# Kernel tuning notes

Measured on AMD Instinct MI355X. Metric: run time of the kernel, lower is better.

The kernel has to match this reference:

```python
import jax, jax.numpy as jnp
import numpy as np

N_NODES = 100000
D_SRC = 128
D_DST = 128
D_OUT = 256
N_EDGES = 600000


def setup_inputs() -> dict:
    key = jax.random.key(0)
    k1, k2, k3, k4, k5 = jax.random.split(key, 5)
    x_src = jax.random.normal(k1, (N_NODES, D_SRC), dtype=jnp.float32)
    x_dst = jax.random.normal(k2, (N_NODES, D_DST), dtype=jnp.float32)
    edge_index = jax.random.randint(k3, (2, N_EDGES), 0, N_NODES, dtype=jnp.int64)
    # Linear(in_src + in_dst, out): torch stores W as [out, in]
    fan_in = D_SRC + D_DST
    bound = 1.0 / np.sqrt(fan_in)
    W = jax.random.uniform(k4, (D_OUT, fan_in), minval=-bound, maxval=bound, dtype=jnp.float32)
    b = jax.random.uniform(k5, (D_OUT,), minval=-bound, maxval=bound, dtype=jnp.float32)
    return {"x_src": x_src, "x_dst": x_dst, "edge_index": edge_index, "W": W, "b": b}


def reference(x_src, x_dst, edge_index, W, b):
    src_idx, dst_idx = edge_index[0], edge_index[1]
    n_dst = x_dst.shape[0]
    x_j = x_src[src_idx]                                  # [E, D_SRC] gather
    summed = jax.ops.segment_sum(x_j, dst_idx, num_segments=n_dst)   # [N, D_SRC]
    count = jax.ops.segment_sum(jnp.ones((src_idx.shape[0],), dtype=x_src.dtype),
                                dst_idx, num_segments=n_dst)          # [N]
    agg = summed / jnp.maximum(count, 1.0)[:, None]        # scatter-mean
    h = jnp.concatenate([x_dst, agg], axis=-1)             # [N, D_DST+D_SRC]
    return jax.nn.relu(h @ W.T + b)                        # [N, D_OUT]
```

## Files before the change

### kernel.cpp

```cpp
#include <hip/hip_runtime.h>

#define N_NODES 100000
#define D_SRC 128
#define D_OUT 256
#define K_DIM 256
#define CAP 32
#define OVF_CAP 2048

typedef __attribute__((ext_vector_type(8))) short short8;
typedef __attribute__((ext_vector_type(4))) float float4v;

__device__ inline unsigned short f2bf(float f) {
    unsigned int u = __float_as_uint(f);
    u += 0x7FFF + ((u >> 16) & 1);
    return (unsigned short)(u >> 16);
}
__device__ inline float bf_lo(unsigned int u) { return __uint_as_float(u << 16); }
__device__ inline float bf_hi(unsigned int u) { return __uint_as_float(u & 0xFFFF0000u); }

__global__ __launch_bounds__(256) void bucket_kernel(
    const int* __restrict__ ei,
    int* __restrict__ deg,
    int* __restrict__ ovf_cnt,
    int* __restrict__ ovf,
    int* __restrict__ bucket,
    int n_edges)
{
    int e = blockIdx.x * 256 + threadIdx.x;
    if (e >= n_edges) return;
    int s = ei[e];
    int d = ei[n_edges + e];
    int pos = atomicAdd(deg + d, 1);
    if (pos < CAP) {
        bucket[(size_t)d * CAP + pos] = s;
    } else {
        int o = atomicAdd(ovf_cnt, 1);
        if (o < OVF_CAP) { ovf[2 * o] = s; ovf[2 * o + 1] = d; }
    }
}

__global__ __launch_bounds__(256) void pack_src_kernel(
    const float* __restrict__ x, unsigned short* __restrict__ xb)
{
    int i = blockIdx.x * 256 + threadIdx.x;
    float4 v = ((const float4*)x)[i];
    ushort4 o;
    o.x = f2bf(v.x); o.y = f2bf(v.y); o.z = f2bf(v.z); o.w = f2bf(v.w);
    ((ushort4*)xb)[i] = o;
}

__global__ __launch_bounds__(256) void pack_dst_sw_kernel(
    const float* __restrict__ x, unsigned short* __restrict__ xdsw)
{
    int t = blockIdx.x * 256 + threadIdx.x;
    int r = t >> 4;
    int g = t & 15;
    const float4* p = (const float4*)(x + (size_t)r * 128 + g * 8);
    float4 v0 = p[0], v1 = p[1];
    union { unsigned short s[8]; short8 v; } pk;
    pk.s[0] = f2bf(v0.x); pk.s[1] = f2bf(v0.y);
    pk.s[2] = f2bf(v0.z); pk.s[3] = f2bf(v0.w);
    pk.s[4] = f2bf(v1.x); pk.s[5] = f2bf(v1.y);
    pk.s[6] = f2bf(v1.z); pk.s[7] = f2bf(v1.w);
    size_t gr = ((size_t)(r >> 4) * 4 + (g >> 2)) * 64 + (r & 15) + ((g & 3) << 4);
    ((short8*)xdsw)[gr] = pk.v;
}

__global__ __launch_bounds__(256) void convert_w_sw_kernel(
    const float* __restrict__ W, unsigned short* __restrict__ wsw)
{
    int t = blockIdx.x * 256 + threadIdx.x;
    int r = t >> 5;
    int g = t & 31;
    const float4* p = (const float4*)(W + (size_t)r * 256 + g * 8);
    float4 v0 = p[0], v1 = p[1];
    union { unsigned short s[8]; short8 v; } pk;
    pk.s[0] = f2bf(v0.x); pk.s[1] = f2bf(v0.y);
    pk.s[2] = f2bf(v0.z); pk.s[3] = f2bf(v0.w);
    pk.s[4] = f2bf(v1.x); pk.s[5] = f2bf(v1.y);
    pk.s[6] = f2bf(v1.z); pk.s[7] = f2bf(v1.w);
    size_t gr = ((size_t)(r >> 4) * 8 + (g >> 2)) * 64 + (r & 15) + ((g & 3) << 4);
    ((short8*)wsw)[gr] = pk.v;
}

__global__ __launch_bounds__(256) void gather_kernel(
    const unsigned short* __restrict__ xsb,
    const int*   __restrict__ deg,
    const int*   __restrict__ bucket,
    const int*   __restrict__ ovf_cnt,
    const int*   __restrict__ ovf,
    unsigned int* __restrict__ aggsw)
{
    int node = blockIdx.x * 4 + (threadIdx.x >> 6);
    if (node >= N_NODES) return;
    int lane = threadIdx.x & 63;

    int dtot = deg[node];
    int n = (dtot < CAP) ? dtot : CAP;

    int idx = bucket[(size_t)node * CAP + (lane & 31)];

    float ax = 0.f, ay = 0.f;
    int i = 0;
    for (; i + 4 <= n; i += 4) {
        int s0 = __shfl(idx, i);
        int s1 = __shfl(idx, i + 1);
        int s2 = __shfl(idx, i + 2);
        int s3 = __shfl(idx, i + 3);
        unsigned int u0 = ((const unsigned int*)(xsb + (size_t)s0 * D_SRC))[lane];
        unsigned int u1 = ((const unsigned int*)(xsb + (size_t)s1 * D_SRC))[lane];
        unsigned int u2 = ((const unsigned int*)(xsb + (size_t)s2 * D_SRC))[lane];
        unsigned int u3 = ((const unsigned int*)(xsb + (size_t)s3 * D_SRC))[lane];
        ax += bf_lo(u0) + bf_lo(u1) + bf_lo(u2) + bf_lo(u3);
        ay += bf_hi(u0) + bf_hi(u1) + bf_hi(u2) + bf_hi(u3);
    }
    for (; i < n; ++i) {
        int s0 = __shfl(idx, i);
        unsigned int u0 = ((const unsigned int*)(xsb + (size_t)s0 * D_SRC))[lane];
        ax += bf_lo(u0);
        ay += bf_hi(u0);
    }

    if (dtot > CAP) {
        int oc = *ovf_cnt;
        if (oc > OVF_CAP) oc = OVF_CAP;
        for (int o = 0; o < oc; ++o) {
            if (ovf[2 * o + 1] == node) {
                int s0 = ovf[2 * o];
                unsigned int u0 = ((const unsigned int*)(xsb + (size_t)s0 * D_SRC))[lane];
                ax += bf_lo(u0);
                ay += bf_hi(u0);
            }
        }
    }

    float inv = 1.0f / (float)((dtot > 1) ? dtot : 1);
    unsigned int packed = (unsigned int)f2bf(ax * inv)
                        | ((unsigned int)f2bf(ay * inv) << 16);
    size_t dw = ((size_t)(node >> 4) * 4 + (lane >> 4)) * 256
              + (size_t)((node & 15) + 16 * ((lane >> 2) & 3)) * 4 + (lane & 3);
    aggsw[dw] = packed;
}

__global__ __launch_bounds__(256) void mfma_gemm_kernel(
    const short8* __restrict__ xdsw,
    const short8* __restrict__ aggsw,
    const short8* __restrict__ wsw,
    const float* __restrict__ bias,
    float*       __restrict__ out)
{
    __shared__ float eps[4][16][68];

    int wave = threadIdx.x >> 6;
    int lane = threadIdx.x & 63;
    int lrow = lane & 15;
    int kq   = lane >> 4;
    int mb   = blockIdx.x;
    int m0   = mb * 64;
    int n0   = wave * 64;

    bool mok[4];
    #pragma unroll
    for (int mf = 0; mf < 4; ++mf) mok[mf] = (m0 + mf * 16) < N_NODES;

    const short8* Ax = xdsw  + (size_t)mb * 1024 + lane;
    const short8* Ag = aggsw + (size_t)mb * 1024 + lane;
    const short8* Bw = wsw   + (size_t)wave * 2048 + lane;

    float4v acc[4][4];
    #pragma unroll
    for (int i = 0; i < 4; ++i)
        #pragma unroll
        for (int j = 0; j < 4; ++j)
            acc[i][j] = (float4v){0.f, 0.f, 0.f, 0.f};

    const short8 zfrag = (short8){0,0,0,0,0,0,0,0};
    short8 a[2][4], b[2][4];

    #pragma unroll
    for (int mf = 0; mf < 4; ++mf)
        a[0][mf] = mok[mf] ? Ax[mf * 256] : zfrag;
    #pragma unroll
    for (int nf = 0; nf < 4; ++nf)
        b[0][nf] = Bw[nf * 512];

    #pragma unroll
    for (int kc = 0; kc < 8; ++kc) {
        const int cur = kc & 1, nxt = cur ^ 1;
        if (kc < 7) {
            const int k1 = kc + 1;
            const short8* A = (k1 < 4) ? Ax : Ag;
            const int kk = (k1 < 4) ? k1 : (k1 - 4);
            #pragma unroll
            for (int mf = 0; mf < 4; ++mf)
                a[nxt][mf] = mok[mf] ? A[mf * 256 + kk * 64] : zfrag;
            #pragma unroll
            for (int nf = 0; nf < 4; ++nf)
                b[nxt][nf] = Bw[nf * 512 + k1 * 64];
        }
        #pragma unroll
        for (int mf = 0; mf < 4; ++mf)
            #pragma unroll
            for (int nf = 0; nf < 4; ++nf)
                acc[mf][nf] = __builtin_amdgcn_mfma_f32_16x16x32_bf16(
                    a[cur][mf], b[cur][nf], acc[mf][nf], 0, 0, 0);
    }

    float bv[4];
    #pragma unroll
    for (int nf = 0; nf < 4; ++nf)
        bv[nf] = bias[n0 + nf * 16 + lrow];

    int srow   = lane >> 4;
    int schunk = lane & 15;

    #pragma unroll
    for (int mf = 0; mf < 4; ++mf) {
        if (!mok[mf]) continue;
        #pragma unroll
        for (int nf = 0; nf < 4; ++nf)
            #pragma unroll
            for (int r = 0; r < 4; ++r)
                eps[wave][kq * 4 + r][nf * 16 + lrow] =
                    fmaxf(acc[mf][nf][r] + bv[nf], 0.f);
        asm volatile("s_waitcnt lgkmcnt(0)" ::: "memory");
        #pragma unroll
        for (int c = 0; c < 4; ++c) {
            int row  = c * 4 + srow;
            float4 v = *(const float4*)&eps[wave][row][schunk * 4];
            int grow = m0 + mf * 16 + row;
            *(float4*)(out + (size_t)grow * D_OUT + n0 + schunk * 4) = v;
        }
        asm volatile("s_waitcnt lgkmcnt(0)" ::: "memory");
    }
}

extern "C" void kernel_launch(void* const* d_in, const int* in_sizes, int n_in,
                              void* d_out, int out_size, void* d_ws, size_t ws_size,
                              hipStream_t stream) {
    const float* x_src = (const float*)d_in[0];
    const float* x_dst = (const float*)d_in[1];
    const int*   ei    = (const int*)d_in[2];
    const float* W     = (const float*)d_in[3];
    const float* bias  = (const float*)d_in[4];
    float* out = (float*)d_out;

    int n_edges = in_sizes[2] / 2;

    int* deg     = (int*)d_ws;
    int* ovf_cnt = deg + N_NODES;
    int* ovf     = ovf_cnt + 4;
    unsigned short* wsw   = (unsigned short*)(ovf + OVF_CAP * 2);
    unsigned short* aggsw = wsw + (size_t)D_OUT * K_DIM;
    unsigned short* xdsw  = aggsw + (size_t)(N_NODES / 16) * 4 * 64 * 8;

    int* bucket = (int*)d_out;
    unsigned short* xsb = (unsigned short*)(bucket + (size_t)N_NODES * CAP);

    hipMemsetAsync(d_ws, 0, (N_NODES + 4) * sizeof(int), stream);

    bucket_kernel<<<(n_edges + 255) / 256, 256, 0, stream>>>(
        ei, deg, ovf_cnt, ovf, bucket, n_edges);

    pack_src_kernel<<<(N_NODES * D_SRC / 4) / 256, 256, 0, stream>>>(x_src, xsb);

    pack_dst_sw_kernel<<<(N_NODES * 16) / 256, 256, 0, stream>>>(x_dst, xdsw);

    convert_w_sw_kernel<<<(D_OUT * K_DIM / 8) / 256, 256, 0, stream>>>(W, wsw);

    gather_kernel<<<(N_NODES + 3) / 4, 256, 0, stream>>>(
        xsb, deg, bucket, ovf_cnt, ovf, (unsigned int*)aggsw);

    mfma_gemm_kernel<<<(N_NODES + 63) / 64, 256, 0, stream>>>(
        (const short8*)xdsw, (const short8*)aggsw, (const short8*)wsw, bias, out);
}
```

Baseline: 314.4 us.

## Merge prep kernels and memset, batch gather loads, use nontemporal output stores

The x_src pack, x_dst swizzled pack, W conversion and degree-counter zeroing now run as one block-partitioned prep kernel, replacing three launches plus a memset. The gather loop issues up to eight predicated row loads before accumulating, to keep more memory requests in flight per wave. The GEMM epilogue writes output with nontemporal stores so the large output stream does not pollute cache. The trade-offs are extra predicated work when degrees are low and possible cache-behaviour shifts, since the output buffer is also reused as scratch earlier in the pipeline.

```diff
diff --git a/kernel.cpp b/kernel.cpp
--- a/kernel.cpp
+++ b/kernel.cpp
@@ -17,6 +17,61 @@
 }
 __device__ inline float bf_lo(unsigned int u) { return __uint_as_float(u << 16); }
 __device__ inline float bf_hi(unsigned int u) { return __uint_as_float(u & 0xFFFF0000u); }
+
+#define PREP_SRC_BLOCKS 12500
+#define PREP_DST_BLOCKS 6250
+#define PREP_W_BLOCKS   32
+#define PREP_Z_BLOCKS   98
+#define PREP_BLOCKS (PREP_SRC_BLOCKS + PREP_DST_BLOCKS + PREP_W_BLOCKS + PREP_Z_BLOCKS)
+
+__global__ __launch_bounds__(256) void prep_kernel(
+    const float* __restrict__ x_src,
+    const float* __restrict__ x_dst,
+    const float* __restrict__ W,
+    unsigned short* __restrict__ xsb,
+    unsigned short* __restrict__ xdsw,
+    unsigned short* __restrict__ wsw,
+    int* __restrict__ deg)
+{
+    int b = blockIdx.x;
+    if (b < PREP_SRC_BLOCKS) {
+        int i = b * 256 + threadIdx.x;
+        float4 v = ((const float4*)x_src)[i];
+        ushort4 o;
+        o.x = f2bf(v.x); o.y = f2bf(v.y); o.z = f2bf(v.z); o.w = f2bf(v.w);
+        ((ushort4*)xsb)[i] = o;
+    } else if (b < PREP_SRC_BLOCKS + PREP_DST_BLOCKS) {
+        int t = (b - PREP_SRC_BLOCKS) * 256 + threadIdx.x;
+        int r = t >> 4;
+        int g = t & 15;
+        const float4* p = (const float4*)(x_dst + (size_t)r * 128 + g * 8);
+        float4 v0 = p[0], v1 = p[1];
+        union { unsigned short s[8]; short8 v; } pk;
+        pk.s[0] = f2bf(v0.x); pk.s[1] = f2bf(v0.y);
+        pk.s[2] = f2bf(v0.z); pk.s[3] = f2bf(v0.w);
+        pk.s[4] = f2bf(v1.x); pk.s[5] = f2bf(v1.y);
+        pk.s[6] = f2bf(v1.z); pk.s[7] = f2bf(v1.w);
+        size_t gr = ((size_t)(r >> 4) * 4 + (g >> 2)) * 64 + (r & 15) + ((g & 3) << 4);
+        ((short8*)xdsw)[gr] = pk.v;
+    } else if (b < PREP_SRC_BLOCKS + PREP_DST_BLOCKS + PREP_W_BLOCKS) {
+        int t = (b - PREP_SRC_BLOCKS - PREP_DST_BLOCKS) * 256 + threadIdx.x;
+        int r = t >> 5;
+        int g = t & 31;
+        const float4* p = (const float4*)(W + (size_t)r * 256 + g * 8);
+        float4 v0 = p[0], v1 = p[1];
+        union { unsigned short s[8]; short8 v; } pk;
+        pk.s[0] = f2bf(v0.x); pk.s[1] = f2bf(v0.y);
+        pk.s[2] = f2bf(v0.z); pk.s[3] = f2bf(v0.w);
+        pk.s[4] = f2bf(v1.x); pk.s[5] = f2bf(v1.y);
+        pk.s[6] = f2bf(v1.z); pk.s[7] = f2bf(v1.w);
+        size_t gr = ((size_t)(r >> 4) * 8 + (g >> 2)) * 64 + (r & 15) + ((g & 3) << 4);
+        ((short8*)wsw)[gr] = pk.v;
+    } else {
+        int i = (b - PREP_SRC_BLOCKS - PREP_DST_BLOCKS - PREP_W_BLOCKS) * 256 + threadIdx.x;
+        if (i < (N_NODES + 4) / 4)
+            ((int4*)deg)[i] = make_int4(0, 0, 0, 0);
+    }
+}
 
 __global__ __launch_bounds__(256) void bucket_kernel(
     const int* __restrict__ ei,
@@ -39,50 +94,6 @@
     }
 }
 
-__global__ __launch_bounds__(256) void pack_src_kernel(
-    const float* __restrict__ x, unsigned short* __restrict__ xb)
-{
-    int i = blockIdx.x * 256 + threadIdx.x;
-    float4 v = ((const float4*)x)[i];
-    ushort4 o;
-    o.x = f2bf(v.x); o.y = f2bf(v.y); o.z = f2bf(v.z); o.w = f2bf(v.w);
-    ((ushort4*)xb)[i] = o;
-}
-
-__global__ __launch_bounds__(256) void pack_dst_sw_kernel(
-    const float* __restrict__ x, unsigned short* __restrict__ xdsw)
-{
-    int t = blockIdx.x * 256 + threadIdx.x;
-    int r = t >> 4;
-    int g = t & 15;
-    const float4* p = (const float4*)(x + (size_t)r * 128 + g * 8);
-    float4 v0 = p[0], v1 = p[1];
-    union { unsigned short s[8]; short8 v; } pk;
-    pk.s[0] = f2bf(v0.x); pk.s[1] = f2bf(v0.y);
-    pk.s[2] = f2bf(v0.z); pk.s[3] = f2bf(v0.w);
-    pk.s[4] = f2bf(v1.x); pk.s[5] = f2bf(v1.y);
-    pk.s[6] = f2bf(v1.z); pk.s[7] = f2bf(v1.w);
-    size_t gr = ((size_t)(r >> 4) * 4 + (g >> 2)) * 64 + (r & 15) + ((g & 3) << 4);
-    ((short8*)xdsw)[gr] = pk.v;
-}
-
-__global__ __launch_bounds__(256) void convert_w_sw_kernel(
-    const float* __restrict__ W, unsigned short* __restrict__ wsw)
-{
-    int t = blockIdx.x * 256 + threadIdx.x;
-    int r = t >> 5;
-    int g = t & 31;
-    const float4* p = (const float4*)(W + (size_t)r * 256 + g * 8);
-    float4 v0 = p[0], v1 = p[1];
-    union { unsigned short s[8]; short8 v; } pk;
-    pk.s[0] = f2bf(v0.x); pk.s[1] = f2bf(v0.y);
-    pk.s[2] = f2bf(v0.z); pk.s[3] = f2bf(v0.w);
-    pk.s[4] = f2bf(v1.x); pk.s[5] = f2bf(v1.y);
-    pk.s[6] = f2bf(v1.z); pk.s[7] = f2bf(v1.w);
-    size_t gr = ((size_t)(r >> 4) * 8 + (g >> 2)) * 64 + (r & 15) + ((g & 3) << 4);
-    ((short8*)wsw)[gr] = pk.v;
-}
-
 __global__ __launch_bounds__(256) void gather_kernel(
     const unsigned short* __restrict__ xsb,
     const int*   __restrict__ deg,
@@ -101,24 +112,22 @@
     int idx = bucket[(size_t)node * CAP + (lane & 31)];
 
     float ax = 0.f, ay = 0.f;
-    int i = 0;
-    for (; i + 4 <= n; i += 4) {
-        int s0 = __shfl(idx, i);
-        int s1 = __shfl(idx, i + 1);
-        int s2 = __shfl(idx, i + 2);
-        int s3 = __shfl(idx, i + 3);
-        unsigned int u0 = ((const unsigned int*)(xsb + (size_t)s0 * D_SRC))[lane];
-        unsigned int u1 = ((const unsigned int*)(xsb + (size_t)s1 * D_SRC))[lane];
-        unsigned int u2 = ((const unsigned int*)(xsb + (size_t)s2 * D_SRC))[lane];
-        unsigned int u3 = ((const unsigned int*)(xsb + (size_t)s3 * D_SRC))[lane];
-        ax += bf_lo(u0) + bf_lo(u1) + bf_lo(u2) + bf_lo(u3);
-        ay += bf_hi(u0) + bf_hi(u1) + bf_hi(u2) + bf_hi(u3);
-    }
-    for (; i < n; ++i) {
-        int s0 = __shfl(idx, i);
-        unsigned int u0 = ((const unsigned int*)(xsb + (size_t)s0 * D_SRC))[lane];
-        ax += bf_lo(u0);
-        ay += bf_hi(u0);
+    for (int base = 0; base < n; base += 8) {
+        unsigned int u[8];
+        #pragma unroll
+        for (int j = 0; j < 8; ++j) {
+            if (base + j < n) {
+                int s = __shfl(idx, base + j);
+                u[j] = ((const unsigned int*)(xsb + (size_t)s * D_SRC))[lane];
+            } else {
+                u[j] = 0;
+            }
+        }
+        #pragma unroll
+        for (int j = 0; j < 8; ++j) {
+            ax += bf_lo(u[j]);
+            ay += bf_hi(u[j]);
+        }
     }
 
     if (dtot > CAP) {
@@ -227,9 +236,10 @@
         #pragma unroll
         for (int c = 0; c < 4; ++c) {
             int row  = c * 4 + srow;
-            float4 v = *(const float4*)&eps[wave][row][schunk * 4];
+            float4v v = *(const float4v*)&eps[wave][row][schunk * 4];
             int grow = m0 + mf * 16 + row;
-            *(float4*)(out + (size_t)grow * D_OUT + n0 + schunk * 4) = v;
+            __builtin_nontemporal_store(v,
+                (float4v*)(out + (size_t)grow * D_OUT + n0 + schunk * 4));
         }
         asm volatile("s_waitcnt lgkmcnt(0)" ::: "memory");
     }
@@ -257,17 +267,12 @@
     int* bucket = (int*)d_out;
     unsigned short* xsb = (unsigned short*)(bucket + (size_t)N_NODES * CAP);
 
-    hipMemsetAsync(d_ws, 0, (N_NODES + 4) * sizeof(int), stream);
+    prep_kernel<<<PREP_BLOCKS, 256, 0, stream>>>(
+        x_src, x_dst, W, xsb, xdsw, wsw, deg);
 
     bucket_kernel<<<(n_edges + 255) / 256, 256, 0, stream>>>(
         ei, deg, ovf_cnt, ovf, bucket, n_edges);
 
-    pack_src_kernel<<<(N_NODES * D_SRC / 4) / 256, 256, 0, stream>>>(x_src, xsb);
-
-    pack_dst_sw_kernel<<<(N_NODES * 16) / 256, 256, 0, stream>>>(x_dst, xdsw);
-
-    convert_w_sw_kernel<<<(D_OUT * K_DIM / 8) / 256, 256, 0, stream>>>(W, wsw);
-
     gather_kernel<<<(N_NODES + 3) / 4, 256, 0, stream>>>(
         xsb, deg, bucket, ovf_cnt, ovf, (unsigned int*)aggsw);
 
```

Result: no change. 318.6 us (+1.3%).
